# Performance work log

Measured on AMD Instinct MI355X. Metric: run time of the kernel, lower is better.

## Reference

```python
import jax, jax.numpy as jnp
import numpy as np

N = 4096      # num_nodes
B = 32        # batch
U = 64        # num_units
L = 2         # num_rnn_layers
K = 2         # max_diffusion_step
OUT = 1       # output_dim (also decoder input_dim)
NM = 2 * K + 1  # num_matrices: 2 supports * K cheb steps + identity


def _random_walk_T(adj):
    # calculate_random_walk_matrix(adj).T : (D^-1 W)^T
    d = adj.sum(axis=1)
    return (adj / d[:, None]).T


def setup_inputs():
    key = jax.random.key(0)
    ks = jax.random.split(key, 16)
    adj = jax.random.uniform(ks[0], (N, N), dtype=jnp.float32)
    S_fwd = _random_walk_T(adj)      # forward transition, transposed
    S_bwd = _random_walk_T(adj.T)    # backward transition, transposed

    inputs = jax.random.normal(ks[1], (B, N, OUT), dtype=jnp.float32)
    hidden_state = jax.random.normal(ks[2], (L, B, N, U), dtype=jnp.float32) * 0.1

    D0 = OUT + U   # layer 0 gconv input width
    D1 = U + U     # layer 1 gconv input width
    s = 0.05
    Wg0 = jax.random.normal(ks[3], (NM * D0, 2 * U), jnp.float32) * s
    bg0 = jnp.ones((2 * U,), jnp.float32)          # bias_start = 1.0 for gates
    Wc0 = jax.random.normal(ks[4], (NM * D0, U), jnp.float32) * s
    bc0 = jnp.zeros((U,), jnp.float32)
    Wg1 = jax.random.normal(ks[5], (NM * D1, 2 * U), jnp.float32) * s
    bg1 = jnp.ones((2 * U,), jnp.float32)
    Wc1 = jax.random.normal(ks[6], (NM * D1, U), jnp.float32) * s
    bc1 = jnp.zeros((U,), jnp.float32)
    Wp = jax.random.normal(ks[7], (U, OUT), jnp.float32) * s
    bp = jnp.zeros((OUT,), jnp.float32)
    return {
        "inputs": inputs, "hidden_state": hidden_state,
        "S_fwd": S_fwd, "S_bwd": S_bwd,
        "Wg0": Wg0, "bg0": bg0, "Wc0": Wc0, "bc0": bc0,
        "Wg1": Wg1, "bg1": bg1, "Wc1": Wc1, "bc1": bc1,
        "Wp": Wp, "bp": bp,
    }


def _gconv(supports, x, h, W, b):
    # diffusion graph convolution with Chebyshev recursion (DCRNN)
    x0 = jnp.concatenate([x, h], axis=-1)      # (B, N, D)
    xs = [x0]
    for S in supports:
        x1 = jnp.einsum('mn,bnd->bmd', S, x0)
        xs.append(x1)
        xk_2, xk_1 = x0, x1
        for _ in range(K - 1):
            x2 = 2.0 * jnp.einsum('mn,bnd->bmd', S, xk_1) - xk_2
            xs.append(x2)
            xk_2, xk_1 = xk_1, x2
    X = jnp.concatenate(xs, axis=-1)           # (B, N, NM*D)
    return X @ W + b


def _dcgru_cell(supports, x, h, Wg, bg, Wc, bc):
    value = jax.nn.sigmoid(_gconv(supports, x, h, Wg, bg))   # (B, N, 2U)
    r, u = jnp.split(value, 2, axis=-1)
    c = jnp.tanh(_gconv(supports, x, r * h, Wc, bc))
    return u * h + (1.0 - u) * c


def reference(inputs, hidden_state, S_fwd, S_bwd,
              Wg0, bg0, Wc0, bc0, Wg1, bg1, Wc1, bc1, Wp, bp):
    supports = (S_fwd, S_bwd)
    layer_params = [(Wg0, bg0, Wc0, bc0), (Wg1, bg1, Wc1, bc1)]
    out = inputs
    new_hidden = []
    for i, (Wg, bg, Wc, bc) in enumerate(layer_params):
        h = _dcgru_cell(supports, out, hidden_state[i], Wg, bg, Wc, bc)
        new_hidden.append(h)
        out = h
    predict = out @ Wp + bp                    # (B, N, OUT)
    return predict, jnp.stack(new_hidden)
```

## Files before the change

### kernel.cpp

```cpp
#include <hip/hip_runtime.h>

typedef unsigned short u16;
typedef unsigned int u32;
typedef unsigned long long u64;
typedef short v8s __attribute__((ext_vector_type(8)));
typedef float v4f __attribute__((ext_vector_type(4)));

#define NN 4096
#define BATCH 32

__device__ __forceinline__ float b2f(u16 u) {
  union { u32 i; float f; } c; c.i = ((u32)u) << 16; return c.f;
}
__device__ __forceinline__ u16 f2b(float f) {
  union { float f; u32 i; } c; c.f = f;
  u32 x = c.i;
  return (u16)((x + 0x7fffu + ((x >> 16) & 1u)) >> 16);
}
__device__ __forceinline__ u32 pk2(float a, float b) {
  return (u32)f2b(a) | ((u32)f2b(b) << 16);
}

typedef const __attribute__((address_space(1))) u32* gp_t;
typedef __attribute__((address_space(3))) u32* lp_t;
__device__ __forceinline__ void gld16(const u16* g, u16* l) {
  __builtin_amdgcn_global_load_lds((gp_t)g, (lp_t)l, 16, 0, 0);
}

#define CBAR() asm volatile("" ::: "memory")
#define BARRIER() do { CBAR(); __builtin_amdgcn_s_barrier(); CBAR(); } while (0)
#define LGKM0() asm volatile("s_waitcnt lgkmcnt(0)" ::: "memory")
#define VMC4() asm volatile("s_waitcnt vmcnt(4)" ::: "memory")
#define VMC3() asm volatile("s_waitcnt vmcnt(3)" ::: "memory")
#define VMC0() asm volatile("s_waitcnt vmcnt(0)" ::: "memory")

__global__ __launch_bounds__(256) void cvtS(const float* __restrict__ S,
                                            u16* __restrict__ Sb) {
  const u64 idx = ((u64)blockIdx.x * 256 + threadIdx.x) * 8;
  const float4 a = *(const float4*)(S + idx);
  const float4 b = *(const float4*)(S + idx + 4);
  uint4 o;
  o.x = pk2(a.x, a.y); o.y = pk2(a.z, a.w);
  o.z = pk2(b.x, b.y); o.w = pk2(b.z, b.w);
  *(uint4*)(Sb + idx) = o;
}

__global__ __launch_bounds__(512, 2) void gemm256(const u16* __restrict__ A,
                                                  const u16* __restrict__ B,
                                                  u16* __restrict__ Ct,
                                                  const u16* __restrict__ Xt) {
  __shared__ __align__(16) u16 lds[65536];
  const int t = threadIdx.x;
  const int wave = t >> 6, lane = t & 63;
  const int q = lane >> 4, r16 = lane & 15;
  const int wm = wave >> 2, wn = wave & 3;

  const int nwg = (int)(gridDim.x * gridDim.y);
  const int bid = (int)(blockIdx.y * gridDim.x + blockIdx.x);
  const int swz = (bid & 7) * (nwg >> 3) + (bid >> 3);
  const int m0 = (swz & 15) << 8;
  const int c0 = (swz >> 4) << 8;

  v4f acc[8][4];
  const v4f vz = {0.f, 0.f, 0.f, 0.f};
#pragma unroll
  for (int i = 0; i < 8; ++i)
#pragma unroll
    for (int j = 0; j < 4; ++j) acc[i][j] = vz;

  const int srow = t >> 3;
  const int sslot = ((t & 7) ^ (srow & 7)) << 3;
  const u16* pA = A + (u64)(m0 + srow) * NN + sslot;
  const u16* pB = B + (u64)(c0 + srow) * NN + sslot;
  const u64 rstep = (u64)64 * NN;
  const u64 hstep = (u64)128 * NN;
  u16* lw = lds + (wave << 9);

  const int sw8 = (q ^ (r16 & 7)) << 3;
  const int aBase = (wm << 13) + (r16 << 6) + sw8;
  const int bBase = 16384 + ((wn >> 1) << 13) + ((wn & 1) << 12) + (r16 << 6) + sw8;

  const int NT = NN >> 6;

  gld16(pA, lw);
  gld16(pA + rstep, lw + 4096);
  gld16(pA + hstep, lw + 8192);
  gld16(pA + hstep + rstep, lw + 12288);
  gld16(pB, lw + 16384);
  gld16(pB + rstep, lw + 20480);
  gld16(pB + hstep, lw + 24576);
  gld16(pB + hstep + rstep, lw + 28672);
  gld16(pB + 64, lw + 32768 + 16384);
  gld16(pB + 64 + rstep, lw + 32768 + 20480);
  gld16(pB + 64 + hstep, lw + 32768 + 24576);
  gld16(pB + 64 + hstep + rstep, lw + 32768 + 28672);
  VMC4();
  BARRIER();

  v8s af[4][2], bf01[2][2], bf23[2][2];
#pragma unroll
  for (int i = 0; i < 4; ++i) {
    const int a = aBase + (i << 10);
    af[i][0] = *(const v8s*)(lds + a);
    af[i][1] = *(const v8s*)(lds + (a ^ 32));
  }
#pragma unroll
  for (int j = 0; j < 2; ++j) {
    const int b = bBase + (j << 10);
    bf01[j][0] = *(const v8s*)(lds + b);
    bf01[j][1] = *(const v8s*)(lds + (b ^ 32));
  }

#pragma unroll 2
  for (int T = 0; T < NT; ++T) {
    const int bo = (T & 1) << 15;
    const int no = bo ^ 32768;
    const u64 ka = (u64)(T + 1 < NT ? T + 1 : NT - 1) << 6;
    const u64 kb = (u64)(T + 2 < NT ? T + 2 : NT - 1) << 6;

    gld16(pA + ka, lw + no);
    gld16(pA + ka + rstep, lw + no + 4096);
#pragma unroll
    for (int j = 0; j < 2; ++j) {
      const int b = bo + bBase + ((2 + j) << 10);
      bf23[j][0] = *(const v8s*)(lds + b);
      bf23[j][1] = *(const v8s*)(lds + (b ^ 32));
    }
    __builtin_amdgcn_s_setprio(1);
#pragma unroll
    for (int i = 0; i < 4; ++i)
#pragma unroll
      for (int j = 0; j < 2; ++j) {
        acc[i][j] = __builtin_amdgcn_mfma_f32_16x16x32_bf16(af[i][0], bf01[j][0], acc[i][j], 0, 0, 0);
        acc[i][j] = __builtin_amdgcn_mfma_f32_16x16x32_bf16(af[i][1], bf01[j][1], acc[i][j], 0, 0, 0);
      }
    __builtin_amdgcn_s_setprio(0);

    gld16(pA + hstep + ka, lw + no + 8192);
    gld16(pA + hstep + ka + rstep, lw + no + 12288);
    LGKM0();
    BARRIER();
    __builtin_amdgcn_s_setprio(1);
#pragma unroll
    for (int i = 0; i < 4; ++i)
#pragma unroll
      for (int j = 0; j < 2; ++j) {
        acc[i][2 + j] = __builtin_amdgcn_mfma_f32_16x16x32_bf16(af[i][0], bf23[j][0], acc[i][2 + j], 0, 0, 0);
        acc[i][2 + j] = __builtin_amdgcn_mfma_f32_16x16x32_bf16(af[i][1], bf23[j][1], acc[i][2 + j], 0, 0, 0);
      }
    __builtin_amdgcn_s_setprio(0);
#pragma unroll
    for (int i = 0; i < 4; ++i) {
      const int a = bo + aBase + ((4 + i) << 10);
      af[i][0] = *(const v8s*)(lds + a);
      af[i][1] = *(const v8s*)(lds + (a ^ 32));
    }
    __builtin_amdgcn_sched_barrier(0);

    gld16(pB + kb, lw + bo + 16384);
    gld16(pB + kb + rstep, lw + bo + 20480);
    __builtin_amdgcn_s_setprio(1);
#pragma unroll
    for (int i = 0; i < 4; ++i)
#pragma unroll
      for (int j = 0; j < 2; ++j) {
        acc[4 + i][2 + j] = __builtin_amdgcn_mfma_f32_16x16x32_bf16(af[i][0], bf23[j][0], acc[4 + i][2 + j], 0, 0, 0);
        acc[4 + i][2 + j] = __builtin_amdgcn_mfma_f32_16x16x32_bf16(af[i][1], bf23[j][1], acc[4 + i][2 + j], 0, 0, 0);
      }
    __builtin_amdgcn_s_setprio(0);

    gld16(pB + hstep + kb, lw + bo + 24576);
    gld16(pB + hstep + kb + rstep, lw + bo + 28672);
    VMC4();
    BARRIER();
    __builtin_amdgcn_s_setprio(1);
#pragma unroll
    for (int i = 0; i < 4; ++i)
#pragma unroll
      for (int j = 0; j < 2; ++j) {
        acc[4 + i][j] = __builtin_amdgcn_mfma_f32_16x16x32_bf16(af[i][0], bf01[j][0], acc[4 + i][j], 0, 0, 0);
        acc[4 + i][j] = __builtin_amdgcn_mfma_f32_16x16x32_bf16(af[i][1], bf01[j][1], acc[4 + i][j], 0, 0, 0);
      }
    __builtin_amdgcn_s_setprio(0);
#pragma unroll
    for (int i = 0; i < 4; ++i) {
      const int a = no + aBase + (i << 10);
      af[i][0] = *(const v8s*)(lds + a);
      af[i][1] = *(const v8s*)(lds + (a ^ 32));
    }
#pragma unroll
    for (int j = 0; j < 2; ++j) {
      const int b = no + bBase + (j << 10);
      bf01[j][0] = *(const v8s*)(lds + b);
      bf01[j][1] = *(const v8s*)(lds + (b ^ 32));
    }
    __builtin_amdgcn_sched_barrier(0);
  }

  VMC0();
  __syncthreads();
#pragma unroll
  for (int i = 0; i < 8; ++i)
#pragma unroll
    for (int j = 0; j < 4; ++j) {
      const int cl = (wn << 6) + (j << 4) + r16;
      const int ml = (wm << 7) + (i << 4) + (q << 2);
      const int phys = (cl << 8) + ((((ml >> 3) ^ (cl & 7)) << 3) | (ml & 7));
      uint2 pv;
      pv.x = pk2(acc[i][j][0], acc[i][j][1]);
      pv.y = pk2(acc[i][j][2], acc[i][j][3]);
      *(uint2*)(lds + phys) = pv;
    }
  __syncthreads();
#pragma unroll
  for (int it = 0; it < 16; ++it) {
    const int f = (it << 9) + t;
    const int cl = f >> 5, sl = f & 31;
    const int phys = (cl << 8) + ((sl ^ (cl & 7)) << 3);
    union { uint4 v; u16 e[8]; } tv;
    tv.v = *(const uint4*)(lds + phys);
    const u64 gi = (u64)(c0 + cl) * NN + m0 + (sl << 3);
    if (Xt) {
      union { uint4 v; u16 e[8]; } xv, ov;
      xv.v = *(const uint4*)(Xt + gi);
#pragma unroll
      for (int s = 0; s < 8; ++s) ov.e[s] = f2b(2.f * b2f(tv.e[s]) - b2f(xv.e[s]));
      *(uint4*)(Ct + gi) = ov.v;
    } else {
      *(uint4*)(Ct + gi) = tv.v;
    }
  }
}

__global__ __launch_bounds__(512, 2) void gemm192(const u16* __restrict__ A,
                                                  const u16* __restrict__ B,
                                                  u16* __restrict__ Ct,
                                                  const u16* __restrict__ Xt) {
  __shared__ __align__(16) u16 lds[57344];
  const int t = threadIdx.x;
  const int wave = t >> 6, lane = t & 63;
  const int q = lane >> 4, r16 = lane & 15;
  const int wm = wave >> 2, wn = wave & 3;

  const int nwg = (int)(gridDim.x * gridDim.y);
  const int bid = (int)(blockIdx.y * gridDim.x + blockIdx.x);
  const int swz = (bid & 7) * (nwg >> 3) + (bid >> 3);
  const int m0 = (swz & 15) << 8;
  const int c0 = (swz >> 4) * 192;

  v4f acc[8][3];
  const v4f vz = {0.f, 0.f, 0.f, 0.f};
#pragma unroll
  for (int i = 0; i < 8; ++i)
#pragma unroll
    for (int j = 0; j < 3; ++j) acc[i][j] = vz;

  const int srow = t >> 3;
  const int sslot = ((t & 7) ^ (srow & 7)) << 3;
  const u16* pA = A + (u64)(m0 + srow) * NN + sslot;
  const u16* pB = B + (u64)(c0 + srow) * NN + sslot;
  const u64 rstep = (u64)64 * NN;
  u16* lw = lds + (wave << 9);

  const int sw8 = (q ^ (r16 & 7)) << 3;
  const int aBase = (wm << 13) + (r16 << 6) + sw8;
  const int bBase = 16384 + wn * 3072 + (r16 << 6) + sw8;

  const int NT = NN >> 6;

  gld16(pA, lw);
  gld16(pA + rstep, lw + 4096);
  gld16(pA + 2 * rstep, lw + 8192);
  gld16(pA + 3 * rstep, lw + 12288);
  gld16(pB, lw + 16384);
  gld16(pB + rstep, lw + 20480);
  gld16(pB + 2 * rstep, lw + 24576);
  gld16(pB + 64, lw + 28672 + 16384);
  gld16(pB + 64 + rstep, lw + 28672 + 20480);
  gld16(pB + 64 + 2 * rstep, lw + 28672 + 24576);
  VMC3();
  BARRIER();

  v8s af[4][2], bf01[2][2], bf2[2];
#pragma unroll
  for (int i = 0; i < 4; ++i) {
    const int a = aBase + (i << 10);
    af[i][0] = *(const v8s*)(lds + a);
    af[i][1] = *(const v8s*)(lds + (a ^ 32));
  }
#pragma unroll
  for (int j = 0; j < 2; ++j) {
    const int b = bBase + (j << 10);
    bf01[j][0] = *(const v8s*)(lds + b);
    bf01[j][1] = *(const v8s*)(lds + (b ^ 32));
  }

#pragma unroll 2
  for (int T = 0; T < NT; ++T) {
    const int bo = (T & 1) ? 28672 : 0;
    const int no = bo ^ 28672;
    const u64 ka = (u64)(T + 1 < NT ? T + 1 : NT - 1) << 6;
    const u64 kb = (u64)(T + 2 < NT ? T + 2 : NT - 1) << 6;

    gld16(pA + ka, lw + no);
    gld16(pA + ka + rstep, lw + no + 4096);
    {
      const int b = bo + bBase + 2048;
      bf2[0] = *(const v8s*)(lds + b);
      bf2[1] = *(const v8s*)(lds + (b ^ 32));
    }
    __builtin_amdgcn_s_setprio(1);
#pragma unroll
    for (int i = 0; i < 4; ++i)
#pragma unroll
      for (int j = 0; j < 2; ++j) {
        acc[i][j] = __builtin_amdgcn_mfma_f32_16x16x32_bf16(af[i][0], bf01[j][0], acc[i][j], 0, 0, 0);
        acc[i][j] = __builtin_amdgcn_mfma_f32_16x16x32_bf16(af[i][1], bf01[j][1], acc[i][j], 0, 0, 0);
      }
    __builtin_amdgcn_s_setprio(0);

    gld16(pA + ka + 2 * rstep, lw + no + 8192);
    gld16(pA + ka + 3 * rstep, lw + no + 12288);
    LGKM0();
    BARRIER();
    __builtin_amdgcn_s_setprio(1);
#pragma unroll
    for (int i = 0; i < 4; ++i) {
      acc[i][2] = __builtin_amdgcn_mfma_f32_16x16x32_bf16(af[i][0], bf2[0], acc[i][2], 0, 0, 0);
      acc[i][2] = __builtin_amdgcn_mfma_f32_16x16x32_bf16(af[i][1], bf2[1], acc[i][2], 0, 0, 0);
    }
    __builtin_amdgcn_s_setprio(0);
#pragma unroll
    for (int i = 0; i < 4; ++i) {
      const int a = bo + aBase + ((4 + i) << 10);
      af[i][0] = *(const v8s*)(lds + a);
      af[i][1] = *(const v8s*)(lds + (a ^ 32));
    }
    __builtin_amdgcn_sched_barrier(0);

    gld16(pB + kb, lw + bo + 16384);
    gld16(pB + kb + rstep, lw + bo + 20480);
    __builtin_amdgcn_s_setprio(1);
#pragma unroll
    for (int i = 0; i < 4; ++i) {
      acc[4 + i][2] = __builtin_amdgcn_mfma_f32_16x16x32_bf16(af[i][0], bf2[0], acc[4 + i][2], 0, 0, 0);
      acc[4 + i][2] = __builtin_amdgcn_mfma_f32_16x16x32_bf16(af[i][1], bf2[1], acc[4 + i][2], 0, 0, 0);
    }
    __builtin_amdgcn_s_setprio(0);

    gld16(pB + kb + 2 * rstep, lw + bo + 24576);
    __builtin_amdgcn_s_setprio(1);
#pragma unroll
    for (int i = 0; i < 4; ++i)
#pragma unroll
      for (int j = 0; j < 2; ++j) {
        acc[4 + i][j] = __builtin_amdgcn_mfma_f32_16x16x32_bf16(af[i][0], bf01[j][0], acc[4 + i][j], 0, 0, 0);
        acc[4 + i][j] = __builtin_amdgcn_mfma_f32_16x16x32_bf16(af[i][1], bf01[j][1], acc[4 + i][j], 0, 0, 0);
      }
    __builtin_amdgcn_s_setprio(0);
    VMC3();
    BARRIER();
#pragma unroll
    for (int i = 0; i < 4; ++i) {
      const int a = no + aBase + (i << 10);
      af[i][0] = *(const v8s*)(lds + a);
      af[i][1] = *(const v8s*)(lds + (a ^ 32));
    }
#pragma unroll
    for (int j = 0; j < 2; ++j) {
      const int b = no + bBase + (j << 10);
      bf01[j][0] = *(const v8s*)(lds + b);
      bf01[j][1] = *(const v8s*)(lds + (b ^ 32));
    }
    __builtin_amdgcn_sched_barrier(0);
  }

  VMC0();
  __syncthreads();
#pragma unroll
  for (int i = 0; i < 8; ++i)
#pragma unroll
    for (int j = 0; j < 3; ++j) {
      const int cl = wn * 48 + j * 16 + r16;
      const int ml = (wm << 7) + (i << 4) + (q << 2);
      const int phys = (cl << 8) + ((((ml >> 3) ^ (cl & 7)) << 3) | (ml & 7));
      uint2 pv;
      pv.x = pk2(acc[i][j][0], acc[i][j][1]);
      pv.y = pk2(acc[i][j][2], acc[i][j][3]);
      *(uint2*)(lds + phys) = pv;
    }
  __syncthreads();
#pragma unroll
  for (int it = 0; it < 12; ++it) {
    const int f = (it << 9) + t;
    const int cl = f >> 5, sl = f & 31;
    const int phys = (cl << 8) + ((sl ^ (cl & 7)) << 3);
    union { uint4 v; u16 e[8]; } tv;
    tv.v = *(const uint4*)(lds + phys);
    const u64 gi = (u64)(c0 + cl) * NN + m0 + (sl << 3);
    if (Xt) {
      union { uint4 v; u16 e[8]; } xv, ov;
      xv.v = *(const uint4*)(Xt + gi);
#pragma unroll
      for (int s = 0; s < 8; ++s) ov.e[s] = f2b(2.f * b2f(tv.e[s]) - b2f(xv.e[s]));
      *(uint4*)(Ct + gi) = ov.v;
    } else {
      *(uint4*)(Ct + gi) = tv.v;
    }
  }
}

__global__ __launch_bounds__(256) void gemm_s(const float* __restrict__ A,
                                              const u16* __restrict__ B,
                                              u16* __restrict__ Ct,
                                              const u16* __restrict__ Xt) {
  __shared__ __align__(16) u16 As[4096];
  __shared__ __align__(16) u16 Bs[4096];
  __shared__ __align__(16) u16 T[16384];
  const int t = threadIdx.x;
  const int wave = t >> 6, lane = t & 63;
  const int m0 = blockIdx.x << 7, c0 = blockIdx.y << 7;
  const int wm = (wave >> 1) << 6, wc = (wave & 1) << 6;
  const int q = lane >> 4, r16 = lane & 15;
  v4f acc[4][4];
  const v4f vz = {0.f, 0.f, 0.f, 0.f};
#pragma unroll
  for (int i = 0; i < 4; ++i)
#pragma unroll
    for (int j = 0; j < 4; ++j) acc[i][j] = vz;

  const int sr = t >> 2;
  const int sc = (t & 3) << 3;
  const u64 abase = (u64)(m0 + sr) * NN + sc;
  const u64 bbase = (u64)(c0 + sr) * NN + sc;
  const u64 rstep = (u64)64 * NN;
  u16* as0 = As + sr * 32 + sc;
  u16* as1 = As + (64 + sr) * 32 + sc;
  u16* bs0 = Bs + sr * 32 + sc;
  u16* bs1 = Bs + (64 + sr) * 32 + sc;

  for (int k0 = 0; k0 < NN; k0 += 32) {
    const float4 a0l = *(const float4*)(A + abase + k0);
    const float4 a0h = *(const float4*)(A + abase + k0 + 4);
    const float4 a1l = *(const float4*)(A + abase + rstep + k0);
    const float4 a1h = *(const float4*)(A + abase + rstep + k0 + 4);
    const uint4 b0 = *(const uint4*)(B + bbase + k0);
    const uint4 b1 = *(const uint4*)(B + bbase + rstep + k0);
    uint4 pa0, pa1;
    pa0.x = pk2(a0l.x, a0l.y); pa0.y = pk2(a0l.z, a0l.w);
    pa0.z = pk2(a0h.x, a0h.y); pa0.w = pk2(a0h.z, a0h.w);
    pa1.x = pk2(a1l.x, a1l.y); pa1.y = pk2(a1l.z, a1l.w);
    pa1.z = pk2(a1h.x, a1h.y); pa1.w = pk2(a1h.z, a1h.w);
    __syncthreads();
    *(uint4*)as0 = pa0;
    *(uint4*)as1 = pa1;
    *(uint4*)bs0 = b0;
    *(uint4*)bs1 = b1;
    __syncthreads();
    v8s af[4], bf[4];
#pragma unroll
    for (int i = 0; i < 4; ++i)
      af[i] = *(const v8s*)(As + ((wm + i * 16 + r16) << 5) + (q << 3));
#pragma unroll
    for (int j = 0; j < 4; ++j)
      bf[j] = *(const v8s*)(Bs + ((wc + j * 16 + r16) << 5) + (q << 3));
#pragma unroll
    for (int i = 0; i < 4; ++i)
#pragma unroll
      for (int j = 0; j < 4; ++j)
        acc[i][j] = __builtin_amdgcn_mfma_f32_16x16x32_bf16(af[i], bf[j], acc[i][j], 0, 0, 0);
  }
#pragma unroll
  for (int i = 0; i < 4; ++i)
#pragma unroll
    for (int j = 0; j < 4; ++j) {
      const int cl = wc + j * 16 + r16;
      const int mm = wm + i * 16 + (q << 2);
      uint2 pv;
      pv.x = pk2(acc[i][j][0], acc[i][j][1]);
      pv.y = pk2(acc[i][j][2], acc[i][j][3]);
      *(uint2*)(T + (cl << 7) + mm) = pv;
    }
  __syncthreads();
#pragma unroll
  for (int it = 0; it < 8; ++it) {
    const int flat = it * 256 + t;
    const int cl = flat >> 4;
    const int seg = (flat & 15) << 3;
    const u64 gi = (u64)(c0 + cl) * NN + m0 + seg;
    union { uint4 v; u16 e[8]; } tv;
    tv.v = *(uint4*)(T + (cl << 7) + seg);
    if (Xt) {
      union { uint4 v; u16 e[8]; } xv, ov;
      xv.v = *(const uint4*)(Xt + gi);
#pragma unroll
      for (int s = 0; s < 8; ++s) ov.e[s] = f2b(2.f * b2f(tv.e[s]) - b2f(xv.e[s]));
      *(uint4*)(Ct + gi) = ov.v;
    } else {
      *(uint4*)(Ct + gi) = tv.v;
    }
  }
}

template <int DP, int KTOT>
__global__ __launch_bounds__(256) void proj_k(const u16* __restrict__ Wt,
                                              const u16* __restrict__ F,
                                              const float* __restrict__ bias,
                                              u16* __restrict__ outp,
                                              const int JSTR, const int ACT) {
  __shared__ __align__(16) u16 As2[2048];
  __shared__ __align__(16) u16 Bs2[4096];
  const int t = threadIdx.x;
  const int wave = t >> 6, lane = t & 63;
  const int q = lane >> 4, r16 = lane & 15;
  const int n0 = blockIdx.x << 7;
  const int j0 = blockIdx.y << 6;
  const int b = blockIdx.z;
  v4f acc[4][2];
  const v4f vz = {0.f, 0.f, 0.f, 0.f};
#pragma unroll
  for (int i = 0; i < 4; ++i) { acc[i][0] = vz; acc[i][1] = vz; }

  const int ar = t >> 2, ac = (t & 3) << 3;
  const u64 wbase = (u64)(j0 + ar) * KTOT + ac;

  for (int k0 = 0; k0 < KTOT; k0 += 32) {
    const uint4 av = *(const uint4*)(Wt + wbase + k0);
    uint4 bv[2];
#pragma unroll
    for (int ci = 0; ci < 2; ++ci) {
      const int c = ci * 256 + t;
      const int kr = c >> 4;
      const int seg = (c & 15) << 3;
      const int kk = k0 + kr;
      const int i = kk / DP;
      const int d = kk - i * DP;
      bv[ci] = *(const uint4*)(F + ((u64)i * (BATCH * DP) + (u64)b * DP + d) * NN + n0 + seg);
    }
    __syncthreads();
    *(uint4*)(As2 + ar * 32 + ac) = av;
#pragma unroll
    for (int ci = 0; ci < 2; ++ci) {
      const int c = ci * 256 + t;
      const int kr = c >> 4;
      const int seg = (c & 15) << 3;
      *(uint4*)(Bs2 + (kr << 7) + seg) = bv[ci];
    }
    __syncthreads();
    v8s af[4], bf[2];
#pragma unroll
    for (int i = 0; i < 4; ++i)
      af[i] = *(const v8s*)(As2 + ((i * 16 + r16) << 5) + (q << 3));
#pragma unroll
    for (int jj = 0; jj < 2; ++jj) {
      const int nn = (wave << 5) + jj * 16 + r16;
      v8s v;
#pragma unroll
      for (int s = 0; s < 8; ++s) v[s] = (short)Bs2[(((q << 3) + s) << 7) + nn];
      bf[jj] = v;
    }
#pragma unroll
    for (int i = 0; i < 4; ++i)
#pragma unroll
      for (int jj = 0; jj < 2; ++jj)
        acc[i][jj] = __builtin_amdgcn_mfma_f32_16x16x32_bf16(af[i], bf[jj], acc[i][jj], 0, 0, 0);
  }
#pragma unroll
  for (int i = 0; i < 4; ++i)
#pragma unroll
    for (int jj = 0; jj < 2; ++jj)
#pragma unroll
      for (int r = 0; r < 4; ++r) {
        const int j = j0 + i * 16 + (q << 2) + r;
        const int n = n0 + (wave << 5) + jj * 16 + r16;
        float v = acc[i][jj][r] + bias[j];
        v = ACT ? (1.f - 2.f / (__expf(2.f * v) + 1.f)) : (1.f / (1.f + __expf(-v)));
        outp[((u64)b * JSTR + j) * NN + n] = f2b(v);
      }
}

__global__ __launch_bounds__(256) void repackW(const float* __restrict__ W, u16* __restrict__ Wt,
                                               const int D, const int DP, const int KTOT,
                                               const int J) {
  const int idx = blockIdx.x * 256 + threadIdx.x;
  if (idx >= J * KTOT) return;
  const int j = idx / KTOT, k = idx - j * KTOT;
  const int i = k / DP, d = k - i * DP;
  u16 v = 0;
  if (i < 5 && d < D) v = f2b(W[(i * D + d) * J + j]);
  Wt[idx] = v;
}

__global__ __launch_bounds__(256) void pack0(const float* __restrict__ x,
                                             const float* __restrict__ hid0,
                                             u16* __restrict__ F0) {
  __shared__ __align__(16) u16 Hs[64 * 72];
  const int b = blockIdx.y, n0 = blockIdx.x << 6, t = threadIdx.x;
  const int r = t >> 2, ds = t & 3;
  const float* hrow = hid0 + ((u64)b * NN + n0 + r) * 64;
#pragma unroll
  for (int c4 = 0; c4 < 4; ++c4) {
    const float4 v = *(const float4*)(hrow + ds * 16 + c4 * 4);
    uint2 p;
    p.x = pk2(v.x, v.y);
    p.y = pk2(v.z, v.w);
    *(uint2*)(Hs + r * 72 + ds * 16 + c4 * 4) = p;
  }
  __syncthreads();
#pragma unroll
  for (int c2 = 0; c2 < 2; ++c2) {
    union { uint4 v; u16 h[8]; } o;
#pragma unroll
    for (int s = 0; s < 8; ++s) o.h[s] = Hs[(ds * 16 + c2 * 8 + s) * 72 + r];
    *(uint4*)(F0 + ((u64)b * 72 + 1 + r) * NN + n0 + ds * 16 + c2 * 8) = o.v;
  }
  if (t < 64) {
    F0[(u64)b * 72 * NN + n0 + t] = f2b(x[(u64)b * NN + n0 + t]);
  } else if (t < 120) {
    const int tt = t - 64;
    const int row = 65 + (tt >> 3), seg = (tt & 7) << 3;
    uint4 z; z.x = z.y = z.z = z.w = 0;
    *(uint4*)(F0 + ((u64)b * 72 + row) * NN + n0 + seg) = z;
  }
}

__global__ __launch_bounds__(256) void pack1(const float* __restrict__ hid1,
                                             u16* __restrict__ F1) {
  __shared__ __align__(16) u16 Hs[64 * 72];
  const int b = blockIdx.y, n0 = blockIdx.x << 6, t = threadIdx.x;
  const int r = t >> 2, ds = t & 3;
  const float* hrow = hid1 + ((u64)b * NN + n0 + r) * 64;
#pragma unroll
  for (int c4 = 0; c4 < 4; ++c4) {
    const float4 v = *(const float4*)(hrow + ds * 16 + c4 * 4);
    uint2 p;
    p.x = pk2(v.x, v.y);
    p.y = pk2(v.z, v.w);
    *(uint2*)(Hs + r * 72 + ds * 16 + c4 * 4) = p;
  }
  __syncthreads();
#pragma unroll
  for (int c2 = 0; c2 < 2; ++c2) {
    union { uint4 v; u16 h[8]; } o;
#pragma unroll
    for (int s = 0; s < 8; ++s) o.h[s] = Hs[(ds * 16 + c2 * 8 + s) * 72 + r];
    *(uint4*)(F1 + ((u64)b * 128 + 64 + r) * NN + n0 + ds * 16 + c2 * 8) = o.v;
  }
}

__global__ __launch_bounds__(256) void candpack(const u16* __restrict__ G, u16* __restrict__ F,
                                                const int DP, const int OFF) {
  const int u = blockIdx.x * 256 + threadIdx.x;
  const int b = u >> 15;
  const int d = (u >> 9) & 63;
  const int seg = (u & 511) << 3;
  union { uint4 v; u16 h[8]; } g, f, o;
  g.v = *(const uint4*)(G + ((u64)b * 128 + d) * NN + seg);
  u16* fp = F + ((u64)b * DP + OFF + d) * NN + seg;
  f.v = *(const uint4*)fp;
#pragma unroll
  for (int s = 0; s < 8; ++s) o.h[s] = f2b(b2f(f.h[s]) * b2f(g.h[s]));
  *(uint4*)fp = o.v;
}

__global__ __launch_bounds__(256) void hnew_k(const u16* __restrict__ G,
                                              const float* __restrict__ hidL,
                                              u16* __restrict__ HnF,
                                              float* __restrict__ outH) {
  __shared__ __align__(16) float Hs[64 * 72];
  __shared__ __align__(16) float T2[64 * 72];
  const int b = blockIdx.y, n0 = blockIdx.x << 6, t = threadIdx.x;
  const int r = t >> 2, ds = t & 3;
  const float* hrow = hidL + ((u64)b * NN + n0 + r) * 64;
#pragma unroll
  for (int c4 = 0; c4 < 4; ++c4)
    *(float4*)(Hs + r * 72 + ds * 16 + c4 * 4) = *(const float4*)(hrow + ds * 16 + c4 * 4);
  __syncthreads();
#pragma unroll
  for (int c2 = 0; c2 < 2; ++c2) {
    const int ncol = ds * 16 + c2 * 8;
    union { uint4 v; u16 h[8]; } uv, cv, o;
    uv.v = *(const uint4*)(G + ((u64)b * 128 + 64 + r) * NN + n0 + ncol);
    cv.v = *(const uint4*)(G + ((u64)b * 128 + r) * NN + n0 + ncol);
#pragma unroll
    for (int s = 0; s < 8; ++s) {
      const int nl = ncol + s;
      const float uu = b2f(uv.h[s]);
      const float hh = Hs[nl * 72 + r];
      const float cc = b2f(cv.h[s]);
      const float v = uu * hh + (1.f - uu) * cc;
      o.h[s] = f2b(v);
      T2[nl * 72 + r] = v;
    }
    *(uint4*)(HnF + ((u64)b * 128 + r) * NN + n0 + ncol) = o.v;
  }
  __syncthreads();
  const int nl2 = t >> 2, dseg = (t & 3) << 4;
#pragma unroll
  for (int c4 = 0; c4 < 4; ++c4) {
    const float4 v = *(const float4*)(T2 + nl2 * 72 + dseg + c4 * 4);
    *(float4*)(outH + ((u64)b * NN + n0 + nl2) * 64 + dseg + c4 * 4) = v;
  }
}

__global__ __launch_bounds__(256) void predictk(const float* __restrict__ H1bnd,
                                                const float* __restrict__ Wp,
                                                const float* __restrict__ bp,
                                                float* __restrict__ outp) {
  __shared__ float w[64];
  __shared__ float bb;
  const int t = threadIdx.x;
  if (t < 64) w[t] = Wp[t];
  if (t == 64) bb = bp[0];
  __syncthreads();
  const int idx = blockIdx.x * 256 + t;
  const float* h = H1bnd + (u64)idx * 64;
  float acc = bb;
#pragma unroll
  for (int c4 = 0; c4 < 16; ++c4) {
    const float4 v = *(const float4*)(h + c4 * 4);
    acc += v.x * w[c4 * 4] + v.y * w[c4 * 4 + 1] + v.z * w[c4 * 4 + 2] + v.w * w[c4 * 4 + 3];
  }
  outp[idx] = acc;
}

extern "C" void kernel_launch(void* const* d_in, const int* in_sizes, int n_in,
                              void* d_out, int out_size, void* d_ws, size_t ws_size,
                              hipStream_t stream) {
  const float* X   = (const float*)d_in[0];
  const float* HID = (const float*)d_in[1];
  const float* Sf  = (const float*)d_in[2];
  const float* Sb  = (const float*)d_in[3];
  const float* Wg0 = (const float*)d_in[4];
  const float* bg0 = (const float*)d_in[5];
  const float* Wc0 = (const float*)d_in[6];
  const float* bc0 = (const float*)d_in[7];
  const float* Wg1 = (const float*)d_in[8];
  const float* bg1 = (const float*)d_in[9];
  const float* Wc1 = (const float*)d_in[10];
  const float* bc1 = (const float*)d_in[11];
  const float* Wp  = (const float*)d_in[12];
  const float* bp  = (const float*)d_in[13];
  float* OUT = (float*)d_out;
  char* ws = (char*)d_ws;

  u16* F = (u16*)(ws);
  u16* G = (u16*)(ws + 167772160ull);
  const u64 NEED_BIG = 167772160ull + 33554432ull + 2ull * 33554432ull + 393216ull;
  const bool big = ws_size >= NEED_BIG;
  u16* Sfb = (u16*)(ws + 167772160ull + 33554432ull);
  u16* Sbb = Sfb + (u64)NN * NN;
  u16* WT = big ? (Sbb + (u64)NN * NN)
                : (u16*)(ws + 167772160ull + 33554432ull);
  u16* Wg0t = WT;
  u16* Wc0t = Wg0t + 128 * 384;
  u16* Wg1t = Wc0t + 64 * 384;
  u16* Wc1t = Wg1t + 128 * 640;

  const float* HID1 = HID + (u64)32 * 4096 * 64;
  float* OUT_H0 = OUT + 131072;
  float* OUT_H1 = OUT + 131072 + 8388608;

  hipMemsetAsync(ws + (u64)11520 * NN * 2, 0, (u64)2304 * NN * 2, stream);

  if (big) {
    cvtS<<<8192, 256, 0, stream>>>(Sf, Sfb);
    cvtS<<<8192, 256, 0, stream>>>(Sb, Sbb);
  }

  repackW<<<(128 * 384 + 255) / 256, 256, 0, stream>>>(Wg0, Wg0t, 65, 72, 384, 128);
  repackW<<<(64 * 384 + 255) / 256, 256, 0, stream>>>(Wc0, Wc0t, 65, 72, 384, 64);
  repackW<<<(128 * 640 + 255) / 256, 256, 0, stream>>>(Wg1, Wg1t, 128, 128, 640, 128);
  repackW<<<(64 * 640 + 255) / 256, 256, 0, stream>>>(Wc1, Wc1t, 128, 128, 640, 64);

  pack0<<<dim3(64, 32), 256, 0, stream>>>(X, HID, F);
  const u64 R0 = (u64)2304 * NN;
  const dim3 g192(16, 12);
  if (big) {
    gemm192<<<g192, 512, 0, stream>>>(Sfb, F, F + R0, nullptr);
    gemm192<<<g192, 512, 0, stream>>>(Sbb, F, F + 3 * R0, nullptr);
    gemm192<<<g192, 512, 0, stream>>>(Sfb, F + R0, F + 2 * R0, F);
    gemm192<<<g192, 512, 0, stream>>>(Sbb, F + 3 * R0, F + 4 * R0, F);
  } else {
    gemm_s<<<dim3(32, 18), 256, 0, stream>>>(Sf, F, F + R0, nullptr);
    gemm_s<<<dim3(32, 18), 256, 0, stream>>>(Sb, F, F + 3 * R0, nullptr);
    gemm_s<<<dim3(32, 18), 256, 0, stream>>>(Sf, F + R0, F + 2 * R0, F);
    gemm_s<<<dim3(32, 18), 256, 0, stream>>>(Sb, F + 3 * R0, F + 4 * R0, F);
  }
  proj_k<72, 384><<<dim3(32, 2, 32), 256, 0, stream>>>(Wg0t, F, bg0, G, 128, 0);
  candpack<<<4096, 256, 0, stream>>>(G, F, 72, 1);
  if (big) {
    gemm192<<<g192, 512, 0, stream>>>(Sfb, F, F + R0, nullptr);
    gemm192<<<g192, 512, 0, stream>>>(Sbb, F, F + 3 * R0, nullptr);
    gemm192<<<g192, 512, 0, stream>>>(Sfb, F + R0, F + 2 * R0, F);
    gemm192<<<g192, 512, 0, stream>>>(Sbb, F + 3 * R0, F + 4 * R0, F);
  } else {
    gemm_s<<<dim3(32, 18), 256, 0, stream>>>(Sf, F, F + R0, nullptr);
    gemm_s<<<dim3(32, 18), 256, 0, stream>>>(Sb, F, F + 3 * R0, nullptr);
    gemm_s<<<dim3(32, 18), 256, 0, stream>>>(Sf, F + R0, F + 2 * R0, F);
    gemm_s<<<dim3(32, 18), 256, 0, stream>>>(Sb, F + 3 * R0, F + 4 * R0, F);
  }
  proj_k<72, 384><<<dim3(32, 1, 32), 256, 0, stream>>>(Wc0t, F, bc0, G, 128, 1);
  hnew_k<<<dim3(64, 32), 256, 0, stream>>>(G, HID, F, OUT_H0);

  pack1<<<dim3(64, 32), 256, 0, stream>>>(HID1, F);
  const u64 R1 = (u64)4096 * NN;
  const dim3 g256(16, 16);
  if (big) {
    gemm256<<<g256, 512, 0, stream>>>(Sfb, F, F + R1, nullptr);
    gemm256<<<g256, 512, 0, stream>>>(Sbb, F, F + 3 * R1, nullptr);
    gemm256<<<g256, 512, 0, stream>>>(Sfb, F + R1, F + 2 * R1, F);
    gemm256<<<g256, 512, 0, stream>>>(Sbb, F + 3 * R1, F + 4 * R1, F);
  } else {
    gemm_s<<<dim3(32, 32), 256, 0, stream>>>(Sf, F, F + R1, nullptr);
    gemm_s<<<dim3(32, 32), 256, 0, stream>>>(Sb, F, F + 3 * R1, nullptr);
    gemm_s<<<dim3(32, 32), 256, 0, stream>>>(Sf, F + R1, F + 2 * R1, F);
    gemm_s<<<dim3(32, 32), 256, 0, stream>>>(Sb, F + 3 * R1, F + 4 * R1, F);
  }
  proj_k<128, 640><<<dim3(32, 2, 32), 256, 0, stream>>>(Wg1t, F, bg1, G, 128, 0);
  candpack<<<4096, 256, 0, stream>>>(G, F, 128, 64);
  if (big) {
    gemm256<<<g256, 512, 0, stream>>>(Sfb, F, F + R1, nullptr);
    gemm256<<<g256, 512, 0, stream>>>(Sbb, F, F + 3 * R1, nullptr);
    gemm256<<<g256, 512, 0, stream>>>(Sfb, F + R1, F + 2 * R1, F);
    gemm256<<<g256, 512, 0, stream>>>(Sbb, F + 3 * R1, F + 4 * R1, F);
  } else {
    gemm_s<<<dim3(32, 32), 256, 0, stream>>>(Sf, F, F + R1, nullptr);
    gemm_s<<<dim3(32, 32), 256, 0, stream>>>(Sb, F, F + 3 * R1, nullptr);
    gemm_s<<<dim3(32, 32), 256, 0, stream>>>(Sf, F + R1, F + 2 * R1, F);
    gemm_s<<<dim3(32, 32), 256, 0, stream>>>(Sb, F + 3 * R1, F + 4 * R1, F);
  }
  proj_k<128, 640><<<dim3(32, 1, 32), 256, 0, stream>>>(Wc1t, F, bc1, G, 128, 1);
  hnew_k<<<dim3(64, 32), 256, 0, stream>>>(G, HID1, F, OUT_H1);

  predictk<<<512, 256, 0, stream>>>(OUT_H1, Wp, bp, OUT);
}
```

Baseline: 1.875 ms.

## Restructure GEMM main loop into 8-phase ping-pong schedule with interleaved wave tiles

Rewrites the 256x256 bf16 GEMM main loop as an explicitly unrolled two-K-tile iteration. Each half-tile load is issued per phase and bracketed by barriers, and the wait threshold changes from vmcnt(4) to vmcnt(6). Wave fragment ownership moves from contiguous 128/64-row blocks to 16-row interleaved strides, and the epilogue index mapping is updated to match. The aim is finer-grained overlap of global-to-LDS loads with MFMA work and possibly fewer LDS bank conflicts. The cost is many more barriers per iteration, which could stall waves.

```diff
diff --git a/kernel.cpp b/kernel.cpp
--- a/kernel.cpp
+++ b/kernel.cpp
@@ -30,7 +30,7 @@
 #define CBAR() asm volatile("" ::: "memory")
 #define BARRIER() do { CBAR(); __builtin_amdgcn_s_barrier(); CBAR(); } while (0)
 #define LGKM0() asm volatile("s_waitcnt lgkmcnt(0)" ::: "memory")
-#define VMC4() asm volatile("s_waitcnt vmcnt(4)" ::: "memory")
+#define VMC6() asm volatile("s_waitcnt vmcnt(6)" ::: "memory")
 #define VMC3() asm volatile("s_waitcnt vmcnt(3)" ::: "memory")
 #define VMC0() asm volatile("s_waitcnt vmcnt(0)" ::: "memory")
 
@@ -77,55 +77,44 @@
   u16* lw = lds + (wave << 9);
 
   const int sw8 = (q ^ (r16 & 7)) << 3;
-  const int aBase = (wm << 13) + (r16 << 6) + sw8;
-  const int bBase = 16384 + ((wn >> 1) << 13) + ((wn & 1) << 12) + (r16 << 6) + sw8;
-
-  const int NT = NN >> 6;
-
-  gld16(pA, lw);
-  gld16(pA + rstep, lw + 4096);
-  gld16(pA + hstep, lw + 8192);
-  gld16(pA + hstep + rstep, lw + 12288);
-  gld16(pB, lw + 16384);
-  gld16(pB + rstep, lw + 20480);
-  gld16(pB + hstep, lw + 24576);
-  gld16(pB + hstep + rstep, lw + 28672);
-  gld16(pB + 64, lw + 32768 + 16384);
-  gld16(pB + 64 + rstep, lw + 32768 + 20480);
+  const int aBase = (((wm << 4) + r16) << 6) + sw8;
+  const int bBase = 16384 + (((wn << 4) + r16) << 6) + sw8;
+
+  gld16(pA, lw);  gld16(pA + rstep, lw + 4096);
+  gld16(pB, lw + 16384);  gld16(pB + rstep, lw + 20480);
+  gld16(pB + hstep, lw + 24576);  gld16(pB + hstep + rstep, lw + 28672);
+  gld16(pA + hstep, lw + 8192);  gld16(pA + hstep + rstep, lw + 12288);
+  gld16(pA + 64, lw + 32768);  gld16(pA + 64 + rstep, lw + 32768 + 4096);
+  gld16(pB + 64, lw + 32768 + 16384);  gld16(pB + 64 + rstep, lw + 32768 + 20480);
   gld16(pB + 64 + hstep, lw + 32768 + 24576);
   gld16(pB + 64 + hstep + rstep, lw + 32768 + 28672);
-  VMC4();
+  VMC6();
   BARRIER();
 
   v8s af[4][2], bf01[2][2], bf23[2][2];
-#pragma unroll
-  for (int i = 0; i < 4; ++i) {
-    const int a = aBase + (i << 10);
-    af[i][0] = *(const v8s*)(lds + a);
-    af[i][1] = *(const v8s*)(lds + (a ^ 32));
-  }
-#pragma unroll
-  for (int j = 0; j < 2; ++j) {
-    const int b = bBase + (j << 10);
-    bf01[j][0] = *(const v8s*)(lds + b);
-    bf01[j][1] = *(const v8s*)(lds + (b ^ 32));
-  }
-
-#pragma unroll 2
-  for (int T = 0; T < NT; ++T) {
-    const int bo = (T & 1) << 15;
-    const int no = bo ^ 32768;
-    const u64 ka = (u64)(T + 1 < NT ? T + 1 : NT - 1) << 6;
-    const u64 kb = (u64)(T + 2 < NT ? T + 2 : NT - 1) << 6;
-
-    gld16(pA + ka, lw + no);
-    gld16(pA + ka + rstep, lw + no + 4096);
+
+#pragma unroll 1
+  for (int it = 0; it < 32; ++it) {
+    const int T = it << 1;
+    const u64 k1 = (u64)(T + 1) << 6;
+    const u64 k2 = (u64)(T + 2 < 64 ? T + 2 : 63) << 6;
+    const u64 k3 = (u64)(T + 3 < 64 ? T + 3 : 63) << 6;
+
+#pragma unroll
+    for (int i = 0; i < 4; ++i) {
+      const int a = aBase + (i << 11);
+      af[i][0] = *(const v8s*)(lds + a);
+      af[i][1] = *(const v8s*)(lds + (a ^ 32));
+    }
 #pragma unroll
     for (int j = 0; j < 2; ++j) {
-      const int b = bo + bBase + ((2 + j) << 10);
-      bf23[j][0] = *(const v8s*)(lds + b);
-      bf23[j][1] = *(const v8s*)(lds + (b ^ 32));
-    }
+      const int b = bBase + (j << 12);
+      bf01[j][0] = *(const v8s*)(lds + b);
+      bf01[j][1] = *(const v8s*)(lds + (b ^ 32));
+    }
+    gld16(pA + hstep + k1, lw + 32768 + 8192);
+    gld16(pA + hstep + rstep + k1, lw + 32768 + 12288);
+    BARRIER(); LGKM0();
     __builtin_amdgcn_s_setprio(1);
 #pragma unroll
     for (int i = 0; i < 4; ++i)
@@ -135,11 +124,17 @@
         acc[i][j] = __builtin_amdgcn_mfma_f32_16x16x32_bf16(af[i][1], bf01[j][1], acc[i][j], 0, 0, 0);
       }
     __builtin_amdgcn_s_setprio(0);
-
-    gld16(pA + hstep + ka, lw + no + 8192);
-    gld16(pA + hstep + ka + rstep, lw + no + 12288);
-    LGKM0();
-    BARRIER();
+    BARRIER();
+
+#pragma unroll
+    for (int j = 0; j < 2; ++j) {
+      const int b = bBase + ((2 + j) << 12);
+      bf23[j][0] = *(const v8s*)(lds + b);
+      bf23[j][1] = *(const v8s*)(lds + (b ^ 32));
+    }
+    gld16(pA + k2, lw);
+    gld16(pA + rstep + k2, lw + 4096);
+    BARRIER(); LGKM0();
     __builtin_amdgcn_s_setprio(1);
 #pragma unroll
     for (int i = 0; i < 4; ++i)
@@ -149,16 +144,17 @@
         acc[i][2 + j] = __builtin_amdgcn_mfma_f32_16x16x32_bf16(af[i][1], bf23[j][1], acc[i][2 + j], 0, 0, 0);
       }
     __builtin_amdgcn_s_setprio(0);
+    BARRIER();
+
 #pragma unroll
     for (int i = 0; i < 4; ++i) {
-      const int a = bo + aBase + ((4 + i) << 10);
+      const int a = aBase + ((4 + i) << 11);
       af[i][0] = *(const v8s*)(lds + a);
       af[i][1] = *(const v8s*)(lds + (a ^ 32));
     }
-    __builtin_amdgcn_sched_barrier(0);
-
-    gld16(pB + kb, lw + bo + 16384);
-    gld16(pB + kb + rstep, lw + bo + 20480);
+    gld16(pB + k2, lw + 16384);
+    gld16(pB + rstep + k2, lw + 20480);
+    BARRIER(); LGKM0();
     __builtin_amdgcn_s_setprio(1);
 #pragma unroll
     for (int i = 0; i < 4; ++i)
@@ -168,10 +164,10 @@
         acc[4 + i][2 + j] = __builtin_amdgcn_mfma_f32_16x16x32_bf16(af[i][1], bf23[j][1], acc[4 + i][2 + j], 0, 0, 0);
       }
     __builtin_amdgcn_s_setprio(0);
-
-    gld16(pB + hstep + kb, lw + bo + 24576);
-    gld16(pB + hstep + kb + rstep, lw + bo + 28672);
-    VMC4();
+    BARRIER();
+
+    gld16(pB + hstep + k2, lw + 24576);
+    gld16(pB + hstep + rstep + k2, lw + 28672);
     BARRIER();
     __builtin_amdgcn_s_setprio(1);
 #pragma unroll
@@ -182,19 +178,89 @@
         acc[4 + i][j] = __builtin_amdgcn_mfma_f32_16x16x32_bf16(af[i][1], bf01[j][1], acc[4 + i][j], 0, 0, 0);
       }
     __builtin_amdgcn_s_setprio(0);
+    VMC6();
+    BARRIER();
+
 #pragma unroll
     for (int i = 0; i < 4; ++i) {
-      const int a = no + aBase + (i << 10);
+      const int a = 32768 + aBase + (i << 11);
       af[i][0] = *(const v8s*)(lds + a);
       af[i][1] = *(const v8s*)(lds + (a ^ 32));
     }
 #pragma unroll
     for (int j = 0; j < 2; ++j) {
-      const int b = no + bBase + (j << 10);
+      const int b = 32768 + bBase + (j << 12);
       bf01[j][0] = *(const v8s*)(lds + b);
       bf01[j][1] = *(const v8s*)(lds + (b ^ 32));
     }
-    __builtin_amdgcn_sched_barrier(0);
+    gld16(pA + hstep + k2, lw + 8192);
+    gld16(pA + hstep + rstep + k2, lw + 12288);
+    BARRIER(); LGKM0();
+    __builtin_amdgcn_s_setprio(1);
+#pragma unroll
+    for (int i = 0; i < 4; ++i)
+#pragma unroll
+      for (int j = 0; j < 2; ++j) {
+        acc[i][j] = __builtin_amdgcn_mfma_f32_16x16x32_bf16(af[i][0], bf01[j][0], acc[i][j], 0, 0, 0);
+        acc[i][j] = __builtin_amdgcn_mfma_f32_16x16x32_bf16(af[i][1], bf01[j][1], acc[i][j], 0, 0, 0);
+      }
+    __builtin_amdgcn_s_setprio(0);
+    BARRIER();
+
+#pragma unroll
+    for (int j = 0; j < 2; ++j) {
+      const int b = 32768 + bBase + ((2 + j) << 12);
+      bf23[j][0] = *(const v8s*)(lds + b);
+      bf23[j][1] = *(const v8s*)(lds + (b ^ 32));
+    }
+    gld16(pA + k3, lw + 32768);
+    gld16(pA + rstep + k3, lw + 32768 + 4096);
+    BARRIER(); LGKM0();
+    __builtin_amdgcn_s_setprio(1);
+#pragma unroll
+    for (int i = 0; i < 4; ++i)
+#pragma unroll
+      for (int j = 0; j < 2; ++j) {
+        acc[i][2 + j] = __builtin_amdgcn_mfma_f32_16x16x32_bf16(af[i][0], bf23[j][0], acc[i][2 + j], 0, 0, 0);
+        acc[i][2 + j] = __builtin_amdgcn_mfma_f32_16x16x32_bf16(af[i][1], bf23[j][1], acc[i][2 + j], 0, 0, 0);
+      }
+    __builtin_amdgcn_s_setprio(0);
+    BARRIER();
+
+#pragma unroll
+    for (int i = 0; i < 4; ++i) {
+      const int a = 32768 + aBase + ((4 + i) << 11);
+      af[i][0] = *(const v8s*)(lds + a);
+      af[i][1] = *(const v8s*)(lds + (a ^ 32));
+    }
+    gld16(pB + k3, lw + 32768 + 16384);
+    gld16(pB + rstep + k3, lw + 32768 + 20480);
+    BARRIER(); LGKM0();
+    __builtin_amdgcn_s_setprio(1);
+#pragma unroll
+    for (int i = 0; i < 4; ++i)
+#pragma unroll
+      for (int j = 0; j < 2; ++j) {
+        acc[4 + i][2 + j] = __builtin_amdgcn_mfma_f32_16x16x32_bf16(af[i][0], bf23[j][0], acc[4 + i][2 + j], 0, 0, 0);
+        acc[4 + i][2 + j] = __builtin_amdgcn_mfma_f32_16x16x32_bf16(af[i][1], bf23[j][1], acc[4 + i][2 + j], 0, 0, 0);
+      }
+    __builtin_amdgcn_s_setprio(0);
+    BARRIER();
+
+    gld16(pB + hstep + k3, lw + 32768 + 24576);
+    gld16(pB + hstep + rstep + k3, lw + 32768 + 28672);
+    BARRIER();
+    __builtin_amdgcn_s_setprio(1);
+#pragma unroll
+    for (int i = 0; i < 4; ++i)
+#pragma unroll
+      for (int j = 0; j < 2; ++j) {
+        acc[4 + i][j] = __builtin_amdgcn_mfma_f32_16x16x32_bf16(af[i][0], bf01[j][0], acc[4 + i][j], 0, 0, 0);
+        acc[4 + i][j] = __builtin_amdgcn_mfma_f32_16x16x32_bf16(af[i][1], bf01[j][1], acc[4 + i][j], 0, 0, 0);
+      }
+    __builtin_amdgcn_s_setprio(0);
+    VMC6();
+    BARRIER();
   }
 
   VMC0();
@@ -203,8 +269,8 @@
   for (int i = 0; i < 8; ++i)
 #pragma unroll
     for (int j = 0; j < 4; ++j) {
-      const int cl = (wn << 6) + (j << 4) + r16;
-      const int ml = (wm << 7) + (i << 4) + (q << 2);
+      const int cl = (j << 6) + (wn << 4) + r16;
+      const int ml = (i << 5) + (wm << 4) + (q << 2);
       const int phys = (cl << 8) + ((((ml >> 3) ^ (cl & 7)) << 3) | (ml & 7));
       uint2 pv;
       pv.x = pk2(acc[i][j][0], acc[i][j][1]);
```

Result: slower. 1.984 ms (+5.8%).
